# Kernel optimization log

Hardware: AMD Instinct MI355X
Metric: run time of the kernel (lower is better)

## Reference

```python
import jax, jax.numpy as jnp
import numpy as np

# Constants mirroring __init__ kwargs
SOURCE_LABEL = 2.0
SINK_LABEL = 3.0
GM_LABEL = 1.0  # hard-coded as `image == 1` in the torch module
THRESH = 0.05
MAX_ITERS = 500


def setup_inputs() -> dict:
    key = jax.random.key(0)
    # Label volume: 0=background, 1=gray matter, 2=source, 3=sink
    image = jax.random.randint(key, (2, 1, 64, 64, 64), 0, 4).astype(jnp.float32)
    return {"image": image}


def _solve(image):
    bs = image.shape[0]
    # squeeze channel, zero-pad each volume by 1 voxel, concat along axis 0
    vol = jnp.pad(image[:, 0], ((0, 0), (1, 1), (1, 1), (1, 1)))  # (bs, D+2, H+2, W+2)
    vol = vol.reshape(-1, vol.shape[2], vol.shape[3])              # (bs*(D+2), H+2, W+2)
    h, w, d = vol.shape
    wopt = 2.0 / (1.0 + np.pi / float(min(h, w, d)))

    # boundary conditions: 0 at source (already 0), 1 at sink
    init = jnp.where(vol == SINK_LABEL, 1.0, 0.0).astype(jnp.float32)

    # red-black coloring restricted to gray-matter voxels
    ii, jj, kk = jnp.meshgrid(jnp.arange(h), jnp.arange(w), jnp.arange(d), indexing="ij")
    parity = (ii + jj + kk) % 2
    gm = (vol == GM_LABEL)
    black = ((parity == 0) & gm).ravel()
    red = ((parity == 1) & gm).ravel()

    flat0 = init.ravel()

    def nbsum(x):
        # flat-index neighbor gathers x[i-1], x[i+1], x[i-d], x[i+d], x[i-d*w], x[i+d*w]
        # roll(x, s)[i] == x[i - s]; colored voxels never sit at flat boundaries
        return (jnp.roll(x, 1) + jnp.roll(x, -1)
                + jnp.roll(x, d) + jnp.roll(x, -d)
                + jnp.roll(x, d * w) + jnp.roll(x, -d * w))

    def half_step(x, mask):
        adj = wopt * (nbsum(x) - 6.0 * x) / 6.0
        x_new = jnp.where(mask, x + adj, x)
        dv = jnp.sum(jnp.abs(jnp.where(mask, adj, 0.0)))
        return x_new, dv

    def body(carry):
        x, it, _ = carry
        x, dv_b = half_step(x, black)   # black sweep uses pre-sweep values
        x, dv_r = half_step(x, red)     # red sweep uses updated black values
        return x, it + 1, dv_b + dv_r

    def cond(carry):
        _, it, dv = carry
        # torch loop breaks when delta_v < thresh or iterations > 500 (checked post-body)
        return (it == 0) | ((dv >= THRESH) & (it <= MAX_ITERS))

    x, iters, dv = jax.lax.while_loop(
        cond, body, (flat0, jnp.int32(0), jnp.float32(0.0)))

    # split concatenated solution back per-volume and crop the padding
    lap = x.reshape(bs, h // bs, w, d)[:, 1:-1, 1:-1, 1:-1][:, None]  # (bs,1,D,H,W)
    return lap, iters, dv


def reference(image):
    return _solve(image)
```

## Files before the change

### kernel.cpp

```cpp
#include <hip/hip_runtime.h>
#include <cstdint>


#define NBLK 132
#define NTHR 1024
#define NW   (NTHR / 64)

constexpr int NJK   = 66;
constexpr int PLANE = 66 * 66;
constexpr int HPL   = PLANE / 2;
constexpr int NI    = 132;
constexpr int CAPL  = 2048;
constexpr int NOUT  = 2 * 64 * 64 * 64;
constexpr int CTRL_U64 = 408 * 16;
constexpr unsigned long long CNT1   = 1ull << 44;
constexpr unsigned long long MASK44 = CNT1 - 1ull;

__global__ void sor_init_ctrl(unsigned long long* ctrl) {
  for (int i = threadIdx.x; i < CTRL_U64; i += blockDim.x) ctrl[i] = 0ull;
}

__device__ __forceinline__ float cloadf(const float* p) {
  return __hip_atomic_load(p, __ATOMIC_RELAXED, __HIP_MEMORY_SCOPE_AGENT);
}
__device__ __forceinline__ void cstoref(float* p, float v) {
  __hip_atomic_store(p, v, __ATOMIC_RELAXED, __HIP_MEMORY_SCOPE_AGENT);
}
__device__ __forceinline__ unsigned long long cloadu(const unsigned long long* p) {
  return __hip_atomic_load(p, __ATOMIC_RELAXED, __HIP_MEMORY_SCOPE_AGENT);
}
__device__ __forceinline__ void cstoreu(unsigned long long* p, unsigned long long v) {
  __hip_atomic_store(p, v, __ATOMIC_RELAXED, __HIP_MEMORY_SCOPE_AGENT);
}

__device__ __forceinline__ int pad_label_idx(int ii, int jj, int kk) {
  int b  = (ii >= 66) ? 1 : 0;
  int pz = ii - 66 * b;
  if (pz < 1 || pz > 64 || jj < 1 || jj > 64 || kk < 1 || kk > 64) return -1;
  return ((b * 64 + (pz - 1)) * 64 + (jj - 1)) * 64 + (kk - 1);
}

__global__ __launch_bounds__(NTHR, 1)
void sor_main(const float* __restrict__ img,
              float* __restrict__ pb0, float* __restrict__ pb1,
              float* __restrict__ pr0, float* __restrict__ pr1,
              unsigned long long* __restrict__ ctrl,
              float* __restrict__ out) {
  __shared__ double P1[PLANE];
  __shared__ unsigned short lsB[CAPL], lsR[CAPL];
  __shared__ unsigned wsum[NW], woff[NW];
  __shared__ unsigned tot;
  __shared__ double redw[NW];
  __shared__ unsigned long long sh_sum;
  __shared__ unsigned long long prevs[8];
  __shared__ double sh_dv;

  const int tid = threadIdx.x, bid = blockIdx.x;
  const int lane = tid & 63, wid = tid >> 6;
  const int z = bid;
  const int zm = (z > 0) ? (z - 1) : z;
  const int zp = (z < NI - 1) ? (z + 1) : z;

  for (int o = tid; o < PLANE; o += NTHR) {
    int j = o / NJK, k = o - j * NJK;
    int li = pad_label_idx(z, j, k);
    float L = (li >= 0) ? img[li] : 0.0f;
    P1[o] = (L == 3.0f) ? 1.0 : 0.0;
  }
  if (tid < 8) prevs[tid] = 0ull;

  int cntB = 0, cntR = 0;
  const int CH = (PLANE + NTHR - 1) / NTHR;
  for (int pass = 0; pass < 2; ++pass) {
    unsigned short* list = (pass == 0) ? lsB : lsR;
    int c0 = tid * CH;
    int c1 = (c0 + CH < PLANE) ? (c0 + CH) : PLANE;
    unsigned cnt = 0;
    for (int o = c0; o < c1; ++o) {
      int j = o / NJK, k = o - j * NJK;
      if (((z + j + k) & 1) != pass) continue;
      int li = pad_label_idx(z, j, k);
      float L = (li >= 0) ? img[li] : 0.0f;
      if (L == 1.0f) cnt++;
    }
    unsigned incl = cnt;
    #pragma unroll
    for (int m = 1; m < 64; m <<= 1) {
      unsigned t = __shfl_up(incl, m, 64);
      if (lane >= m) incl += t;
    }
    __syncthreads();
    if (lane == 63) wsum[wid] = incl;
    __syncthreads();
    if (tid == 0) {
      unsigned a = 0;
      for (int w = 0; w < NW; ++w) { unsigned c = wsum[w]; woff[w] = a; a += c; }
      tot = a;
    }
    __syncthreads();
    unsigned p = (incl - cnt) + woff[wid];
    for (int o = c0; o < c1; ++o) {
      int j = o / NJK, k = o - j * NJK;
      if (((z + j + k) & 1) != pass) continue;
      int li = pad_label_idx(z, j, k);
      float L = (li >= 0) ? img[li] : 0.0f;
      if (L == 1.0f) list[p++] = (unsigned short)o;
    }
    __syncthreads();
    if (pass == 0) cntB = (int)tot; else cntR = (int)tot;
  }

  auto publishHalf = [&](float* dst, int cb) {
    for (int c = tid; c < HPL; c += NTHR) {
      int j = c / 33, m = c - 33 * j;
      int k = (m << 1) + ((z + j + cb) & 1);
      cstoref(&dst[c], (float)P1[NJK * j + k]);
    }
  };

  const double WOPT = 2.0 / (1.0 + 3.14159265358979323846 / 66.0);

  publishHalf(pr0 + (size_t)z * HPL, 1);
  __syncthreads();
  if (tid == 0)
    __hip_atomic_fetch_add(&ctrl[(128u + (unsigned)(bid & 15)) * 16u], 1ull,
                           __ATOMIC_RELAXED, __HIP_MEMORY_SCOPE_AGENT);
  if (tid < 16) {
    for (;;) {
      unsigned long long v = cloadu(&ctrl[(128u + (unsigned)tid) * 16u]);
      v += __shfl_xor(v, 1, 64);  v += __shfl_xor(v, 2, 64);
      v += __shfl_xor(v, 4, 64);  v += __shfl_xor(v, 8, 64);
      if (v >= (unsigned long long)NBLK) break;
      __builtin_amdgcn_s_sleep(1);
    }
  }
  __syncthreads();

  int itout = 0;
  double dvout = 0.0;

  for (int t = 1; t <= 555; ++t) {
    const float* __restrict__ prold = (t & 1) ? pr0 : pr1;
    float* __restrict__ pbcur       = (t & 1) ? pb1 : pb0;
    float* __restrict__ prcur       = (t & 1) ? pr1 : pr0;

    if (t > 1) {
      if (tid < 2) {
        int nz = (tid == 0) ? (z - 1) : (z + 1);
        if (nz >= 0 && nz < NI) {
          while (cloadu(&ctrl[(276u + (unsigned)nz) * 16u])
                 < (unsigned long long)(t - 1))
            __builtin_amdgcn_s_sleep(1);
        }
      }
      __syncthreads();
    }

    double acc = 0.0;
    {
      const float* __restrict__ rm = prold + (size_t)zm * HPL;
      const float* __restrict__ rp = prold + (size_t)zp * HPL;
      for (int p = tid; p < cntB; p += NTHR) {
        const int o = (int)lsB[p];
        int j = o / NJK, k = o - j * NJK;
        int c = 33 * j + (k >> 1);
        float fzm = cloadf(&rm[c]);
        float fzp = cloadf(&rp[c]);
        double xi = P1[o];
        double nb = ((((P1[o - 1] + P1[o + 1]) + P1[o - NJK]) + P1[o + NJK])
                    + (double)fzm) + (double)fzp;
        double adj = (WOPT * (nb - 6.0 * xi)) / 6.0;
        P1[o] = xi + adj;
        acc += fabs(adj);
      }
    }
    __syncthreads();
    publishHalf(pbcur + (size_t)z * HPL, 0);
    __syncthreads();
    if (tid == 0)
      cstoreu(&ctrl[(144u + (unsigned)z) * 16u], (unsigned long long)t);
    if (tid < 2) {
      int nz = (tid == 0) ? (z - 1) : (z + 1);
      if (nz >= 0 && nz < NI) {
        while (cloadu(&ctrl[(144u + (unsigned)nz) * 16u])
               < (unsigned long long)t)
          __builtin_amdgcn_s_sleep(1);
      }
    }
    __syncthreads();

    {
      const float* __restrict__ bm = pbcur + (size_t)zm * HPL;
      const float* __restrict__ bp = pbcur + (size_t)zp * HPL;
      for (int p = tid; p < cntR; p += NTHR) {
        const int o = (int)lsR[p];
        int j = o / NJK, k = o - j * NJK;
        int c = 33 * j + (k >> 1);
        float fzm = cloadf(&bm[c]);
        float fzp = cloadf(&bp[c]);
        double xi = P1[o];
        double nb = ((((P1[o - 1] + P1[o + 1]) + P1[o - NJK]) + P1[o + NJK])
                    + (double)fzm) + (double)fzp;
        double adj = (WOPT * (nb - 6.0 * xi)) / 6.0;
        P1[o] = xi + adj;
        acc += fabs(adj);
      }
    }
    __syncthreads();
    publishHalf(prcur + (size_t)z * HPL, 1);

    double a = acc;
    #pragma unroll
    for (int m = 32; m >= 1; m >>= 1) a += __shfl_xor(a, m, 64);
    if (lane == 0) redw[wid] = a;
    __syncthreads();
    if (tid == 0) {
      double s = redw[0];
      #pragma unroll
      for (int w = 1; w < NW; ++w) s += redw[w];
      cstoreu(&ctrl[(276u + (unsigned)z) * 16u], (unsigned long long)t);
      __hip_atomic_fetch_add(
          &ctrl[(((unsigned)t & 7u) * 16u + (unsigned)(bid & 15)) * 16u],
          CNT1 + (unsigned long long)(s * 1048576.0 + 0.5),
          __ATOMIC_RELAXED, __HIP_MEMORY_SCOPE_AGENT);
    }

    const int g = t - 2;
    if (g >= 1) {
      const int r = g & 7;
      const unsigned n = ((unsigned)g + 7u) >> 3;
      if (tid < 16) {
        const unsigned long long t64 =
            ((unsigned long long)(132u * n)) << 44;
        for (;;) {
          unsigned long long v =
              cloadu(&ctrl[((unsigned)r * 16u + (unsigned)tid) * 16u]);
          v += __shfl_xor(v, 1, 64);  v += __shfl_xor(v, 2, 64);
          v += __shfl_xor(v, 4, 64);  v += __shfl_xor(v, 8, 64);
          if (v >= t64) { if (tid == 0) sh_sum = v; break; }
          __builtin_amdgcn_s_sleep(1);
        }
      }
      __syncthreads();
      if (tid == 0) {
        unsigned long long cum = sh_sum & MASK44;
        sh_dv = (double)(cum - prevs[r]) * (1.0 / 1048576.0);
        prevs[r] = cum;
      }
      __syncthreads();
      double dvg = sh_dv;
      if (!((dvg >= 0.05) && (g <= 500))) { itout = g; dvout = dvg; break; }
    }
  }

  {
    const int vb = (z >= 66) ? 1 : 0;
    const int pz = z - 66 * vb;
    if (pz >= 1 && pz <= 64) {
      float* ob = out + ((size_t)vb * 64 + (pz - 1)) * 4096;
      for (int t2 = tid; t2 < 4096; t2 += NTHR) {
        int jj = t2 >> 6, kk = t2 & 63;
        ob[t2] = (float)P1[NJK * (jj + 1) + (kk + 1)];
      }
    }
    if (z == 0 && tid == 0) {
      out[NOUT]     = (float)itout;
      out[NOUT + 1] = (float)dvout;
    }
  }
}

extern "C" void kernel_launch(void* const* d_in, const int* in_sizes, int n_in,
                              void* d_out, int out_size, void* d_ws, size_t ws_size,
                              hipStream_t stream) {
  const float* img = (const float*)d_in[0];
  float* out = (float*)d_out;
  float* pb0 = (float*)d_ws;
  float* pb1 = pb0 + (size_t)NI * HPL;
  float* pr0 = pb1 + (size_t)NI * HPL;
  float* pr1 = pr0 + (size_t)NI * HPL;
  unsigned long long* ctrl = (unsigned long long*)(pr1 + (size_t)NI * HPL);

  sor_init_ctrl<<<1, 256, 0, stream>>>(ctrl);
  sor_main<<<NBLK, NTHR, 0, stream>>>(img, pb0, pb1, pr0, pr1, ctrl, out);
}
```

Measured before the change: 653.3 us.

## Fuse half-plane publish into sweeps and merge convergence check with neighbor wait

Each updated gray-matter voxel is now written straight to the global exchange buffer inside the sweep loop. This replaces the separate full half-plane publish pass and one barrier per half-sweep. Since only gray-matter voxels change, all four exchange buffers are seeded once at startup. The lagged convergence poll now runs in a second wavefront at the same time as the neighbor-plane wait at the top of the next iteration, which removes two block barriers per iteration. Precomputed compressed-plane indices are packed into the voxel lists, doubling their LDS footprint, to avoid a per-voxel division.

```diff
diff --git a/kernel.cpp b/kernel.cpp
--- a/kernel.cpp
+++ b/kernel.cpp
@@ -47,11 +47,10 @@
               unsigned long long* __restrict__ ctrl,
               float* __restrict__ out) {
   __shared__ double P1[PLANE];
-  __shared__ unsigned short lsB[CAPL], lsR[CAPL];
+  __shared__ unsigned lsB[CAPL], lsR[CAPL];
   __shared__ unsigned wsum[NW], woff[NW];
   __shared__ unsigned tot;
   __shared__ double redw[NW];
-  __shared__ unsigned long long sh_sum;
   __shared__ unsigned long long prevs[8];
   __shared__ double sh_dv;
 
@@ -72,7 +71,7 @@
   int cntB = 0, cntR = 0;
   const int CH = (PLANE + NTHR - 1) / NTHR;
   for (int pass = 0; pass < 2; ++pass) {
-    unsigned short* list = (pass == 0) ? lsB : lsR;
+    unsigned* list = (pass == 0) ? lsB : lsR;
     int c0 = tid * CH;
     int c1 = (c0 + CH < PLANE) ? (c0 + CH) : PLANE;
     unsigned cnt = 0;
@@ -104,23 +103,24 @@
       if (((z + j + k) & 1) != pass) continue;
       int li = pad_label_idx(z, j, k);
       float L = (li >= 0) ? img[li] : 0.0f;
-      if (L == 1.0f) list[p++] = (unsigned short)o;
+      if (L == 1.0f)
+        list[p++] = (unsigned)o | ((unsigned)(33 * j + (k >> 1)) << 16);
     }
     __syncthreads();
     if (pass == 0) cntB = (int)tot; else cntR = (int)tot;
   }
 
-  auto publishHalf = [&](float* dst, int cb) {
-    for (int c = tid; c < HPL; c += NTHR) {
-      int j = c / 33, m = c - 33 * j;
-      int k = (m << 1) + ((z + j + cb) & 1);
-      cstoref(&dst[c], (float)P1[NJK * j + k]);
-    }
-  };
-
-  const double WOPT = 2.0 / (1.0 + 3.14159265358979323846 / 66.0);
-
-  publishHalf(pr0 + (size_t)z * HPL, 1);
+  for (int c = tid; c < HPL; c += NTHR) {
+    int j = c / 33, m = c - 33 * j;
+    int kb = (m << 1) + ((z + j) & 1);
+    int kr = (m << 1) + ((z + j + 1) & 1);
+    float vb = (float)P1[NJK * j + kb];
+    float vr = (float)P1[NJK * j + kr];
+    cstoref(&pb0[(size_t)z * HPL + c], vb);
+    cstoref(&pb1[(size_t)z * HPL + c], vb);
+    cstoref(&pr0[(size_t)z * HPL + c], vr);
+    cstoref(&pr1[(size_t)z * HPL + c], vr);
+  }
   __syncthreads();
   if (tid == 0)
     __hip_atomic_fetch_add(&ctrl[(128u + (unsigned)(bid & 15)) * 16u], 1ull,
@@ -136,6 +136,8 @@
   }
   __syncthreads();
 
+  const double WOPT = 2.0 / (1.0 + 3.14159265358979323846 / 66.0);
+
   int itout = 0;
   double dvout = 0.0;
 
@@ -145,37 +147,62 @@
     float* __restrict__ prcur       = (t & 1) ? pr1 : pr0;
 
     if (t > 1) {
-      if (tid < 2) {
-        int nz = (tid == 0) ? (z - 1) : (z + 1);
+      const int g = t - 2;
+      if (wid == 0 && lane < 2) {
+        int nz = (lane == 0) ? (z - 1) : (z + 1);
         if (nz >= 0 && nz < NI) {
           while (cloadu(&ctrl[(276u + (unsigned)nz) * 16u])
                  < (unsigned long long)(t - 1))
             __builtin_amdgcn_s_sleep(1);
         }
       }
+      if (g >= 1 && wid == 1 && lane < 16) {
+        const int r = g & 7;
+        const unsigned n = ((unsigned)g + 7u) >> 3;
+        const unsigned long long t64 =
+            ((unsigned long long)(132u * n)) << 44;
+        unsigned long long v;
+        for (;;) {
+          v = cloadu(&ctrl[((unsigned)r * 16u + (unsigned)lane) * 16u]);
+          v += __shfl_xor(v, 1, 64);  v += __shfl_xor(v, 2, 64);
+          v += __shfl_xor(v, 4, 64);  v += __shfl_xor(v, 8, 64);
+          if (v >= t64) break;
+          __builtin_amdgcn_s_sleep(1);
+        }
+        if (lane == 0) {
+          unsigned long long cum = v & MASK44;
+          sh_dv = (double)(cum - prevs[r]) * (1.0 / 1048576.0);
+          prevs[r] = cum;
+        }
+      }
       __syncthreads();
+      if (g >= 1) {
+        double dvg = sh_dv;
+        if (!((dvg >= 0.05) && (g <= 500))) { itout = g; dvout = dvg; break; }
+      }
     }
 
     double acc = 0.0;
     {
       const float* __restrict__ rm = prold + (size_t)zm * HPL;
       const float* __restrict__ rp = prold + (size_t)zp * HPL;
+      float* __restrict__ pbz = pbcur + (size_t)z * HPL;
       for (int p = tid; p < cntB; p += NTHR) {
-        const int o = (int)lsB[p];
-        int j = o / NJK, k = o - j * NJK;
-        int c = 33 * j + (k >> 1);
+        const unsigned e = lsB[p];
+        const int o = (int)(e & 0xFFFFu);
+        const int c = (int)(e >> 16);
         float fzm = cloadf(&rm[c]);
         float fzp = cloadf(&rp[c]);
         double xi = P1[o];
         double nb = ((((P1[o - 1] + P1[o + 1]) + P1[o - NJK]) + P1[o + NJK])
                     + (double)fzm) + (double)fzp;
         double adj = (WOPT * (nb - 6.0 * xi)) / 6.0;
-        P1[o] = xi + adj;
+        double v = xi + adj;
+        P1[o] = v;
+        cstoref(&pbz[c], (float)v);
         acc += fabs(adj);
       }
     }
-    __syncthreads();
-    publishHalf(pbcur + (size_t)z * HPL, 0);
     __syncthreads();
     if (tid == 0)
       cstoreu(&ctrl[(144u + (unsigned)z) * 16u], (unsigned long long)t);
@@ -192,22 +219,23 @@
     {
       const float* __restrict__ bm = pbcur + (size_t)zm * HPL;
       const float* __restrict__ bp = pbcur + (size_t)zp * HPL;
+      float* __restrict__ prz = prcur + (size_t)z * HPL;
       for (int p = tid; p < cntR; p += NTHR) {
-        const int o = (int)lsR[p];
-        int j = o / NJK, k = o - j * NJK;
-        int c = 33 * j + (k >> 1);
+        const unsigned e = lsR[p];
+        const int o = (int)(e & 0xFFFFu);
+        const int c = (int)(e >> 16);
         float fzm = cloadf(&bm[c]);
         float fzp = cloadf(&bp[c]);
         double xi = P1[o];
         double nb = ((((P1[o - 1] + P1[o + 1]) + P1[o - NJK]) + P1[o + NJK])
                     + (double)fzm) + (double)fzp;
         double adj = (WOPT * (nb - 6.0 * xi)) / 6.0;
-        P1[o] = xi + adj;
+        double v = xi + adj;
+        P1[o] = v;
+        cstoref(&prz[c], (float)v);
         acc += fabs(adj);
       }
     }
-    __syncthreads();
-    publishHalf(prcur + (size_t)z * HPL, 1);
 
     double a = acc;
     #pragma unroll
@@ -223,33 +251,6 @@
           &ctrl[(((unsigned)t & 7u) * 16u + (unsigned)(bid & 15)) * 16u],
           CNT1 + (unsigned long long)(s * 1048576.0 + 0.5),
           __ATOMIC_RELAXED, __HIP_MEMORY_SCOPE_AGENT);
-    }
-
-    const int g = t - 2;
-    if (g >= 1) {
-      const int r = g & 7;
-      const unsigned n = ((unsigned)g + 7u) >> 3;
-      if (tid < 16) {
-        const unsigned long long t64 =
-            ((unsigned long long)(132u * n)) << 44;
-        for (;;) {
-          unsigned long long v =
-              cloadu(&ctrl[((unsigned)r * 16u + (unsigned)tid) * 16u]);
-          v += __shfl_xor(v, 1, 64);  v += __shfl_xor(v, 2, 64);
-          v += __shfl_xor(v, 4, 64);  v += __shfl_xor(v, 8, 64);
-          if (v >= t64) { if (tid == 0) sh_sum = v; break; }
-          __builtin_amdgcn_s_sleep(1);
-        }
-      }
-      __syncthreads();
-      if (tid == 0) {
-        unsigned long long cum = sh_sum & MASK44;
-        sh_dv = (double)(cum - prevs[r]) * (1.0 / 1048576.0);
-        prevs[r] = cum;
-      }
-      __syncthreads();
-      double dvg = sh_dv;
-      if (!((dvg >= 0.05) && (g <= 500))) { itout = g; dvout = dvg; break; }
     }
   }
 
```

After: 523.9 us. 19.8% less time.

## Exchange only compacted GM-to-GM halo values between neighbouring plane blocks

Applied to the files above, without the earlier changes.

Each block used to publish a full half-plane of values to global memory every sweep. Now it precomputes, per colored voxel, compact slot indices for gray-matter neighbours in the adjacent planes. Only those values are written straight from the update loop into per-interface slots, and neighbours stage them into shared memory before the sweep. Non-GM neighbours are encoded as constants (0 or 1 for sink). The convergence wait is moved to the start of the next iteration and run in a separate wavefront, alongside the neighbour wait, to cut barrier count. In exchange it uses more shared memory and adds extra setup passes over the labels.

```diff
diff --git a/kernel.cpp b/kernel.cpp
--- a/kernel.cpp
+++ b/kernel.cpp
@@ -8,9 +8,10 @@
 
 constexpr int NJK   = 66;
 constexpr int PLANE = 66 * 66;
-constexpr int HPL   = PLANE / 2;
 constexpr int NI    = 132;
 constexpr int CAPL  = 2048;
+constexpr int SLOT  = 768;
+constexpr int NIF   = 133;
 constexpr int NOUT  = 2 * 64 * 64 * 64;
 constexpr int CTRL_U64 = 408 * 16;
 constexpr unsigned long long CNT1   = 1ull << 44;
@@ -47,19 +48,20 @@
               unsigned long long* __restrict__ ctrl,
               float* __restrict__ out) {
   __shared__ double P1[PLANE];
+  __shared__ unsigned short tmpm[PLANE];
+  __shared__ unsigned short tmpp[PLANE];
   __shared__ unsigned short lsB[CAPL], lsR[CAPL];
+  __shared__ unsigned auxB[CAPL], auxR[CAPL];
+  __shared__ float HM[SLOT], HP[SLOT];
   __shared__ unsigned wsum[NW], woff[NW];
   __shared__ unsigned tot;
   __shared__ double redw[NW];
-  __shared__ unsigned long long sh_sum;
   __shared__ unsigned long long prevs[8];
   __shared__ double sh_dv;
 
   const int tid = threadIdx.x, bid = blockIdx.x;
   const int lane = tid & 63, wid = tid >> 6;
   const int z = bid;
-  const int zm = (z > 0) ? (z - 1) : z;
-  const int zp = (z < NI - 1) ? (z + 1) : z;
 
   for (int o = tid; o < PLANE; o += NTHR) {
     int j = o / NJK, k = o - j * NJK;
@@ -69,19 +71,22 @@
   }
   if (tid < 8) prevs[tid] = 0ull;
 
-  int cntB = 0, cntR = 0;
   const int CH = (PLANE + NTHR - 1) / NTHR;
-  for (int pass = 0; pass < 2; ++pass) {
-    unsigned short* list = (pass == 0) ? lsB : lsR;
+  int nM = 0, nP = 0;
+  for (int dir = 0; dir < 2; ++dir) {
+    const int zx = (dir == 0) ? (z - 1) : (z + 1);
+    unsigned short* tmp = (dir == 0) ? tmpm : tmpp;
     int c0 = tid * CH;
     int c1 = (c0 + CH < PLANE) ? (c0 + CH) : PLANE;
     unsigned cnt = 0;
     for (int o = c0; o < c1; ++o) {
       int j = o / NJK, k = o - j * NJK;
-      if (((z + j + k) & 1) != pass) continue;
       int li = pad_label_idx(z, j, k);
       float L = (li >= 0) ? img[li] : 0.0f;
-      if (L == 1.0f) cnt++;
+      if (L != 1.0f) continue;
+      int lx = pad_label_idx(zx, j, k);
+      float Lx = (lx >= 0) ? img[lx] : 0.0f;
+      if (Lx == 1.0f) cnt++;
     }
     unsigned incl = cnt;
     #pragma unroll
@@ -101,26 +106,80 @@
     unsigned p = (incl - cnt) + woff[wid];
     for (int o = c0; o < c1; ++o) {
       int j = o / NJK, k = o - j * NJK;
-      if (((z + j + k) & 1) != pass) continue;
       int li = pad_label_idx(z, j, k);
       float L = (li >= 0) ? img[li] : 0.0f;
-      if (L == 1.0f) list[p++] = (unsigned short)o;
-    }
-    __syncthreads();
-    if (pass == 0) cntB = (int)tot; else cntR = (int)tot;
-  }
-
-  auto publishHalf = [&](float* dst, int cb) {
-    for (int c = tid; c < HPL; c += NTHR) {
-      int j = c / 33, m = c - 33 * j;
-      int k = (m << 1) + ((z + j + cb) & 1);
-      cstoref(&dst[c], (float)P1[NJK * j + k]);
-    }
-  };
-
-  const double WOPT = 2.0 / (1.0 + 3.14159265358979323846 / 66.0);
-
-  publishHalf(pr0 + (size_t)z * HPL, 1);
+      if (L != 1.0f) continue;
+      int lx = pad_label_idx(zx, j, k);
+      float Lx = (lx >= 0) ? img[lx] : 0.0f;
+      if (Lx == 1.0f) tmp[o] = (unsigned short)(p++);
+    }
+    __syncthreads();
+    if (dir == 0) nM = (int)tot; else nP = (int)tot;
+  }
+
+  int cntB = 0, cntR = 0;
+  for (int cb = 0; cb < 2; ++cb) {
+    unsigned short* list = (cb == 0) ? lsB : lsR;
+    unsigned* aux        = (cb == 0) ? auxB : auxR;
+    int c0 = tid * CH;
+    int c1 = (c0 + CH < PLANE) ? (c0 + CH) : PLANE;
+    unsigned cnt = 0;
+    for (int o = c0; o < c1; ++o) {
+      int j = o / NJK, k = o - j * NJK;
+      if (((z + j + k) & 1) != cb) continue;
+      int li = pad_label_idx(z, j, k);
+      float L = (li >= 0) ? img[li] : 0.0f;
+      if (L == 1.0f) cnt++;
+    }
+    unsigned incl = cnt;
+    #pragma unroll
+    for (int m = 1; m < 64; m <<= 1) {
+      unsigned t = __shfl_up(incl, m, 64);
+      if (lane >= m) incl += t;
+    }
+    __syncthreads();
+    if (lane == 63) wsum[wid] = incl;
+    __syncthreads();
+    if (tid == 0) {
+      unsigned a = 0;
+      for (int w = 0; w < NW; ++w) { unsigned c = wsum[w]; woff[w] = a; a += c; }
+      tot = a;
+    }
+    __syncthreads();
+    unsigned p = (incl - cnt) + woff[wid];
+    for (int o = c0; o < c1; ++o) {
+      int j = o / NJK, k = o - j * NJK;
+      if (((z + j + k) & 1) != cb) continue;
+      int li = pad_label_idx(z, j, k);
+      float L = (li >= 0) ? img[li] : 0.0f;
+      if (L != 1.0f) continue;
+      int lm = pad_label_idx(z - 1, j, k);
+      float Lm = (lm >= 0) ? img[lm] : 0.0f;
+      int lp = pad_label_idx(z + 1, j, k);
+      float Lp = (lp >= 0) ? img[lp] : 0.0f;
+      unsigned cm = (Lm == 1.0f) ? (unsigned)tmpm[o]
+                                 : (0x8000u | (Lm == 3.0f ? 1u : 0u));
+      unsigned cp = (Lp == 1.0f) ? (unsigned)tmpp[o]
+                                 : (0x8000u | (Lp == 3.0f ? 1u : 0u));
+      list[p] = (unsigned short)o;
+      aux[p]  = cm | (cp << 16);
+      p++;
+    }
+    __syncthreads();
+    if (cb == 0) cntB = (int)tot; else cntR = (int)tot;
+  }
+
+  const size_t offRm = ((size_t)z * 2 + 0) * SLOT;
+  const size_t offPm = ((size_t)z * 2 + 1) * SLOT;
+  const size_t offRp = ((size_t)(z + 1) * 2 + 1) * SLOT;
+  const size_t offPp = ((size_t)(z + 1) * 2 + 0) * SLOT;
+
+  for (int p = tid; p < cntR; p += NTHR) {
+    unsigned u = auxR[p];
+    unsigned cm = u & 0xFFFFu, cp = u >> 16;
+    if (!(cm & 0x8000u)) cstoref(&pr0[offPm + cm], 0.0f);
+    if (!(cp & 0x8000u)) cstoref(&pr0[offPp + cp], 0.0f);
+  }
   __syncthreads();
   if (tid == 0)
     __hip_atomic_fetch_add(&ctrl[(128u + (unsigned)(bid & 15)) * 16u], 1ull,
@@ -136,6 +195,8 @@
   }
   __syncthreads();
 
+  const double WOPT = 2.0 / (1.0 + 3.14159265358979323846 / 66.0);
+
   int itout = 0;
   double dvout = 0.0;
 
@@ -145,69 +206,101 @@
     float* __restrict__ prcur       = (t & 1) ? pr1 : pr0;
 
     if (t > 1) {
-      if (tid < 2) {
-        int nz = (tid == 0) ? (z - 1) : (z + 1);
-        if (nz >= 0 && nz < NI) {
-          while (cloadu(&ctrl[(276u + (unsigned)nz) * 16u])
+      const int g = t - 2;
+      if (wid == 0 && lane < 2) {
+        int nb = (lane == 0) ? (bid - 1) : (bid + 1);
+        if (nb >= 0 && nb < NBLK) {
+          while (cloadu(&ctrl[(276u + (unsigned)nb) * 16u])
                  < (unsigned long long)(t - 1))
             __builtin_amdgcn_s_sleep(1);
         }
       }
+      if (g >= 1 && wid == 1 && lane < 16) {
+        const int r = g & 7;
+        const unsigned n = ((unsigned)g + 7u) >> 3;
+        const unsigned long long t64 =
+            ((unsigned long long)NBLK * n) << 44;
+        unsigned long long v;
+        for (;;) {
+          v = cloadu(&ctrl[((unsigned)r * 16u + (unsigned)lane) * 16u]);
+          v += __shfl_xor(v, 1, 64);  v += __shfl_xor(v, 2, 64);
+          v += __shfl_xor(v, 4, 64);  v += __shfl_xor(v, 8, 64);
+          if (v >= t64) break;
+          __builtin_amdgcn_s_sleep(1);
+        }
+        if (lane == 0) {
+          unsigned long long cum = v & MASK44;
+          sh_dv = (double)(cum - prevs[r]) * (1.0 / 1048576.0);
+          prevs[r] = cum;
+        }
+      }
       __syncthreads();
+      if (g >= 1) {
+        double dvg = sh_dv;
+        if (!((dvg >= 0.05) && (g <= 500))) { itout = g; dvout = dvg; break; }
+      }
     }
 
     double acc = 0.0;
+    if (tid < nM) HM[tid] = cloadf(&prold[offRm + tid]);
+    if (tid < nP) HP[tid] = cloadf(&prold[offRp + tid]);
+    __syncthreads();
     {
-      const float* __restrict__ rm = prold + (size_t)zm * HPL;
-      const float* __restrict__ rp = prold + (size_t)zp * HPL;
+      float* __restrict__ wm = pbcur + offPm;
+      float* __restrict__ wp = pbcur + offPp;
       for (int p = tid; p < cntB; p += NTHR) {
         const int o = (int)lsB[p];
-        int j = o / NJK, k = o - j * NJK;
-        int c = 33 * j + (k >> 1);
-        float fzm = cloadf(&rm[c]);
-        float fzp = cloadf(&rp[c]);
+        const unsigned u = auxB[p];
+        const unsigned cm = u & 0xFFFFu, cp = u >> 16;
+        double fzm = (cm & 0x8000u) ? (double)(cm & 1u) : (double)HM[cm];
+        double fzp = (cp & 0x8000u) ? (double)(cp & 1u) : (double)HP[cp];
         double xi = P1[o];
         double nb = ((((P1[o - 1] + P1[o + 1]) + P1[o - NJK]) + P1[o + NJK])
-                    + (double)fzm) + (double)fzp;
+                    + fzm) + fzp;
         double adj = (WOPT * (nb - 6.0 * xi)) / 6.0;
-        P1[o] = xi + adj;
+        double v = xi + adj;
+        P1[o] = v;
+        if (!(cm & 0x8000u)) cstoref(&wm[cm], (float)v);
+        if (!(cp & 0x8000u)) cstoref(&wp[cp], (float)v);
         acc += fabs(adj);
       }
     }
     __syncthreads();
-    publishHalf(pbcur + (size_t)z * HPL, 0);
-    __syncthreads();
     if (tid == 0)
-      cstoreu(&ctrl[(144u + (unsigned)z) * 16u], (unsigned long long)t);
+      cstoreu(&ctrl[(144u + (unsigned)bid) * 16u], (unsigned long long)t);
     if (tid < 2) {
-      int nz = (tid == 0) ? (z - 1) : (z + 1);
-      if (nz >= 0 && nz < NI) {
-        while (cloadu(&ctrl[(144u + (unsigned)nz) * 16u])
+      int nb = (tid == 0) ? (bid - 1) : (bid + 1);
+      if (nb >= 0 && nb < NBLK) {
+        while (cloadu(&ctrl[(144u + (unsigned)nb) * 16u])
                < (unsigned long long)t)
           __builtin_amdgcn_s_sleep(1);
       }
     }
     __syncthreads();
 
+    if (tid < nM) HM[tid] = cloadf(&pbcur[offRm + tid]);
+    if (tid < nP) HP[tid] = cloadf(&pbcur[offRp + tid]);
+    __syncthreads();
     {
-      const float* __restrict__ bm = pbcur + (size_t)zm * HPL;
-      const float* __restrict__ bp = pbcur + (size_t)zp * HPL;
+      float* __restrict__ wm = prcur + offPm;
+      float* __restrict__ wp = prcur + offPp;
       for (int p = tid; p < cntR; p += NTHR) {
         const int o = (int)lsR[p];
-        int j = o / NJK, k = o - j * NJK;
-        int c = 33 * j + (k >> 1);
-        float fzm = cloadf(&bm[c]);
-        float fzp = cloadf(&bp[c]);
+        const unsigned u = auxR[p];
+        const unsigned cm = u & 0xFFFFu, cp = u >> 16;
+        double fzm = (cm & 0x8000u) ? (double)(cm & 1u) : (double)HM[cm];
+        double fzp = (cp & 0x8000u) ? (double)(cp & 1u) : (double)HP[cp];
         double xi = P1[o];
         double nb = ((((P1[o - 1] + P1[o + 1]) + P1[o - NJK]) + P1[o + NJK])
-                    + (double)fzm) + (double)fzp;
+                    + fzm) + fzp;
         double adj = (WOPT * (nb - 6.0 * xi)) / 6.0;
-        P1[o] = xi + adj;
+        double v = xi + adj;
+        P1[o] = v;
+        if (!(cm & 0x8000u)) cstoref(&wm[cm], (float)v);
+        if (!(cp & 0x8000u)) cstoref(&wp[cp], (float)v);
         acc += fabs(adj);
       }
     }
-    __syncthreads();
-    publishHalf(prcur + (size_t)z * HPL, 1);
 
     double a = acc;
     #pragma unroll
@@ -218,38 +311,11 @@
       double s = redw[0];
       #pragma unroll
       for (int w = 1; w < NW; ++w) s += redw[w];
-      cstoreu(&ctrl[(276u + (unsigned)z) * 16u], (unsigned long long)t);
+      cstoreu(&ctrl[(276u + (unsigned)bid) * 16u], (unsigned long long)t);
       __hip_atomic_fetch_add(
           &ctrl[(((unsigned)t & 7u) * 16u + (unsigned)(bid & 15)) * 16u],
           CNT1 + (unsigned long long)(s * 1048576.0 + 0.5),
           __ATOMIC_RELAXED, __HIP_MEMORY_SCOPE_AGENT);
-    }
-
-    const int g = t - 2;
-    if (g >= 1) {
-      const int r = g & 7;
-      const unsigned n = ((unsigned)g + 7u) >> 3;
-      if (tid < 16) {
-        const unsigned long long t64 =
-            ((unsigned long long)(132u * n)) << 44;
-        for (;;) {
-          unsigned long long v =
-              cloadu(&ctrl[((unsigned)r * 16u + (unsigned)tid) * 16u]);
-          v += __shfl_xor(v, 1, 64);  v += __shfl_xor(v, 2, 64);
-          v += __shfl_xor(v, 4, 64);  v += __shfl_xor(v, 8, 64);
-          if (v >= t64) { if (tid == 0) sh_sum = v; break; }
-          __builtin_amdgcn_s_sleep(1);
-        }
-      }
-      __syncthreads();
-      if (tid == 0) {
-        unsigned long long cum = sh_sum & MASK44;
-        sh_dv = (double)(cum - prevs[r]) * (1.0 / 1048576.0);
-        prevs[r] = cum;
-      }
-      __syncthreads();
-      double dvg = sh_dv;
-      if (!((dvg >= 0.05) && (g <= 500))) { itout = g; dvout = dvg; break; }
     }
   }
 
@@ -275,11 +341,12 @@
                               hipStream_t stream) {
   const float* img = (const float*)d_in[0];
   float* out = (float*)d_out;
+  const size_t CH_ELEMS = (size_t)NIF * 2 * SLOT;
   float* pb0 = (float*)d_ws;
-  float* pb1 = pb0 + (size_t)NI * HPL;
-  float* pr0 = pb1 + (size_t)NI * HPL;
-  float* pr1 = pr0 + (size_t)NI * HPL;
-  unsigned long long* ctrl = (unsigned long long*)(pr1 + (size_t)NI * HPL);
+  float* pb1 = pb0 + CH_ELEMS;
+  float* pr0 = pb1 + CH_ELEMS;
+  float* pr1 = pr0 + CH_ELEMS;
+  unsigned long long* ctrl = (unsigned long long*)(pr1 + CH_ELEMS);
 
   sor_init_ctrl<<<1, 256, 0, stream>>>(ctrl);
   sor_main<<<NBLK, NTHR, 0, stream>>>(img, pb0, pb1, pr0, pr1, ctrl, out);
```

Measured after the change: 663.6 us. Within noise of the previous version (+1.6%).
